# Optimization experiments

Measured on AMD Instinct MI355X. Metric: run time of the kernel, lower is better.

## Reference

```python
import jax, jax.numpy as jnp
import numpy as np

B, N, DIM = 2, 1024, 256
DEPTH, HEADS, DIM_HEAD = 4, 4, 64
INNER = HEADS * DIM_HEAD
SCALE = DIM_HEAD ** -0.5
STEP, LAMBD, EPS = 0.1, 0.1, 1e-5


def cx(re, im):
    return jax.lax.complex(re, im)


def setup_inputs() -> dict:
    key = jax.random.key(0)
    ks = jax.random.split(key, 8)
    s = np.float32(1.0 / np.sqrt(DIM))
    f32 = jnp.float32
    return {
        "x_re": jax.random.normal(ks[0], (B, N, DIM), f32),
        "x_im": jax.random.normal(ks[1], (B, N, DIM), f32),
        "ln1_w_re": jnp.ones((DEPTH, DIM), f32),
        "ln1_w_im": jnp.zeros((DEPTH, DIM), f32),
        "ln1_b_re": jnp.zeros((DEPTH, DIM), f32),
        "ln1_b_im": jnp.zeros((DEPTH, DIM), f32),
        "qkv_re": jax.random.normal(ks[2], (DEPTH, INNER, DIM), f32) * s,
        "qkv_im": jax.random.normal(ks[3], (DEPTH, INNER, DIM), f32) * s,
        "out_w_re": jax.random.normal(ks[4], (DEPTH, DIM, INNER), f32) * s,
        "out_w_im": jax.random.normal(ks[5], (DEPTH, DIM, INNER), f32) * s,
        "out_b_re": jnp.zeros((DEPTH, DIM), f32),
        "out_b_im": jnp.zeros((DEPTH, DIM), f32),
        "ln2_w_re": jnp.ones((DEPTH, DIM), f32),
        "ln2_w_im": jnp.zeros((DEPTH, DIM), f32),
        "ln2_b_re": jnp.zeros((DEPTH, DIM), f32),
        "ln2_b_im": jnp.zeros((DEPTH, DIM), f32),
        "ff_re": jax.random.normal(ks[6], (DEPTH, DIM, DIM), f32) * s,
        "ff_im": jax.random.normal(ks[7], (DEPTH, DIM, DIM), f32) * s,
    }


def complex_layernorm(x, w, b):
    # per-component mean/var on real and imag (torch unbiased=False), complex sqrt
    mean = cx(jnp.mean(x.real, -1, keepdims=True), jnp.mean(x.imag, -1, keepdims=True))
    var = cx(jnp.var(x.real, -1, keepdims=True), jnp.var(x.imag, -1, keepdims=True))
    xn = (x - mean) / jnp.sqrt(var + EPS)
    return w * xn + b


def attention(x, Wqkv, Wout, bout):
    # torch Linear: y = x @ W^T ; shared qkv projection w
    w = jnp.einsum('bnd,ed->bne', x, Wqkv)              # [B,N,INNER]
    w = w.reshape(B, N, HEADS, DIM_HEAD).transpose(0, 2, 1, 3)  # [B,H,N,Dh]
    dots = jnp.einsum('bhnd,bhmd->bhnm', w, w.conj()) * SCALE   # complex scores
    mag = jnp.abs(dots)
    a = jax.nn.softmax(mag, axis=-1)                    # softmax on magnitudes
    ph = jnp.angle(dots)                                # polar reconstruction
    attn = cx(a * jnp.cos(ph), a * jnp.sin(ph))
    out = jnp.einsum('bhnm,bhmd->bhnd', attn, w)
    out = out.transpose(0, 2, 1, 3).reshape(B, N, INNER)
    return jnp.einsum('bne,de->bnd', out, Wout) + bout


def feedforward(x, W):
    # FeedForward type1: x1 = x W^T ; CReLU(x + step*x1 - step*lambd)
    x1 = jnp.einsum('bnd,ed->bne', x, W)
    z = x + STEP * x1 - STEP * LAMBD
    return cx(jax.nn.relu(z.real), jax.nn.relu(z.imag))


def reference(x_re, x_im, ln1_w_re, ln1_w_im, ln1_b_re, ln1_b_im,
              qkv_re, qkv_im, out_w_re, out_w_im, out_b_re, out_b_im,
              ln2_w_re, ln2_w_im, ln2_b_re, ln2_b_im, ff_re, ff_im):
    x = cx(x_re, x_im)
    for l in range(DEPTH):
        xn = complex_layernorm(x, cx(ln1_w_re[l], ln1_w_im[l]), cx(ln1_b_re[l], ln1_b_im[l]))
        grad_x = attention(xn, cx(qkv_re[l], qkv_im[l]), cx(out_w_re[l], out_w_im[l]),
                           cx(out_b_re[l], out_b_im[l])) + x
        xn2 = complex_layernorm(grad_x, cx(ln2_w_re[l], ln2_w_im[l]), cx(ln2_b_re[l], ln2_b_im[l]))
        x = feedforward(xn2, cx(ff_re[l], ff_im[l]))
    return x
```

## Files before the change

kernel.cpp:

```cpp
#include <hip/hip_runtime.h>
#include <math.h>

#define B_ 2
#define N_ 1024
#define DIM_ 256
#define DEPTH_ 4
#define HEADS_ 4
#define DHEAD_ 64
#define INNER_ 256
#define SCALE_ 0.125f
#define STEP_ 0.1f
#define LAMBD_ 0.1f
#define EPS_ 1e-5f

typedef __attribute__((ext_vector_type(8))) short short8;
typedef __attribute__((ext_vector_type(4))) float f32x4;

__device__ __forceinline__ unsigned short bf16_rne(float x) {
    unsigned u = __float_as_uint(x);
    unsigned r = (u + 0x7FFFu + ((u >> 16) & 1u)) >> 16;
    return (unsigned short)r;
}
__device__ __forceinline__ float bf16_tof(unsigned short h) {
    return __uint_as_float(((unsigned)h) << 16);
}
__device__ __forceinline__ void split2(float x, unsigned short& hi, unsigned short& lo) {
    hi = bf16_rne(x);
    lo = bf16_rne(x - bf16_tof(hi));
}
__device__ __forceinline__ f32x4 mfma16(short8 a, short8 b, f32x4 c) {
    return __builtin_amdgcn_mfma_f32_16x16x32_bf16(a, b, c, 0, 0, 0);
}
__device__ __forceinline__ short8 neg8(short8 v) {
    union { short8 s; unsigned u[4]; } a; a.s = v;
    a.u[0] ^= 0x80008000u; a.u[1] ^= 0x80008000u;
    a.u[2] ^= 0x80008000u; a.u[3] ^= 0x80008000u;
    return a.s;
}

__global__ __launch_bounds__(64)
void ln_kernel(const float* __restrict__ xr, const float* __restrict__ xi,
               const float* __restrict__ wr, const float* __restrict__ wi,
               const float* __restrict__ br, const float* __restrict__ bi,
               float* __restrict__ outr, float* __restrict__ outi,
               unsigned short* __restrict__ planes, int S) {
    int row = blockIdx.x;
    int lane = threadIdx.x;
    int base = row * DIM_ + lane * 4;

    float4 xr4 = *(const float4*)(xr + base);
    float4 xi4 = *(const float4*)(xi + base);
    float ar[4] = {xr4.x, xr4.y, xr4.z, xr4.w};
    float ai[4] = {xi4.x, xi4.y, xi4.z, xi4.w};

    float sr = ar[0] + ar[1] + ar[2] + ar[3];
    float si = ai[0] + ai[1] + ai[2] + ai[3];
#pragma unroll
    for (int o = 1; o < 64; o <<= 1) {
        sr += __shfl_xor(sr, o, 64);
        si += __shfl_xor(si, o, 64);
    }
    float mre = sr * (1.f / DIM_), mim = si * (1.f / DIM_);

    float drv[4], div[4];
    float vr = 0.f, vi = 0.f;
#pragma unroll
    for (int j = 0; j < 4; j++) {
        drv[j] = ar[j] - mre;
        div[j] = ai[j] - mim;
        vr += drv[j] * drv[j];
        vi += div[j] * div[j];
    }
#pragma unroll
    for (int o = 1; o < 64; o <<= 1) {
        vr += __shfl_xor(vr, o, 64);
        vi += __shfl_xor(vi, o, 64);
    }
    float c = vr * (1.f / DIM_) + EPS_;
    float d = vi * (1.f / DIM_);
    float r = sqrtf(c * c + d * d);
    float sre = sqrtf(0.5f * (r + c));
    float sim = sqrtf(fmaxf(0.5f * (r - c), 0.f));
    float inv = 1.f / r;

    int wc = lane * 4;
    float4 wr4 = *(const float4*)(wr + wc);
    float4 wi4 = *(const float4*)(wi + wc);
    float4 br4 = *(const float4*)(br + wc);
    float4 bi4 = *(const float4*)(bi + wc);
    float wrv[4] = {wr4.x, wr4.y, wr4.z, wr4.w};
    float wiv[4] = {wi4.x, wi4.y, wi4.z, wi4.w};
    float brv[4] = {br4.x, br4.y, br4.z, br4.w};
    float biv[4] = {bi4.x, bi4.y, bi4.z, bi4.w};

    float orr[4], oii[4];
    unsigned short rh[4], rl[4], ih[4], il[4];
#pragma unroll
    for (int j = 0; j < 4; j++) {
        float nr = (drv[j] * sre + div[j] * sim) * inv;
        float ni = (div[j] * sre - drv[j] * sim) * inv;
        orr[j] = wrv[j] * nr - wiv[j] * ni + brv[j];
        oii[j] = wrv[j] * ni + wiv[j] * nr + biv[j];
        split2(orr[j], rh[j], rl[j]);
        split2(oii[j], ih[j], il[j]);
    }
    *(float4*)(outr + base) = make_float4(orr[0], orr[1], orr[2], orr[3]);
    *(float4*)(outi + base) = make_float4(oii[0], oii[1], oii[2], oii[3]);
    *(ushort4*)(planes + 0 * (size_t)S + base) = make_ushort4(rh[0], rh[1], rh[2], rh[3]);
    *(ushort4*)(planes + 1 * (size_t)S + base) = make_ushort4(rl[0], rl[1], rl[2], rl[3]);
    *(ushort4*)(planes + 2 * (size_t)S + base) = make_ushort4(ih[0], ih[1], ih[2], ih[3]);
    *(ushort4*)(planes + 3 * (size_t)S + base) = make_ushort4(il[0], il[1], il[2], il[3]);
}

__global__ void wsplit_all(const float* __restrict__ s0r, const float* __restrict__ s0i,
                           const float* __restrict__ s1r, const float* __restrict__ s1i,
                           const float* __restrict__ s2r, const float* __restrict__ s2i,
                           unsigned short* __restrict__ d0,
                           unsigned short* __restrict__ d1,
                           unsigned short* __restrict__ d2) {
    const int PER = DEPTH_ * 65536;
    int gid = blockIdx.x * 256 + threadIdx.x;
    int sel = gid / PER;
    int idx = gid - sel * PER;
    const float* wr = (sel == 0) ? s0r : (sel == 1) ? s1r : s2r;
    const float* wi = (sel == 0) ? s0i : (sel == 1) ? s1i : s2i;
    unsigned short* dst = (sel == 0) ? d0 : (sel == 1) ? d1 : d2;
    int l = idx >> 16, e = idx & 65535;
    unsigned short rh, rl, ih, il;
    split2(wr[idx], rh, rl);
    split2(wi[idx], ih, il);
    size_t base = (size_t)l * 4 * 65536;
    dst[base + 0 * 65536 + e] = rh;
    dst[base + 1 * 65536 + e] = rl;
    dst[base + 2 * 65536 + e] = ih;
    dst[base + 3 * 65536 + e] = il;
}

template <int MODE>
__global__ __launch_bounds__(256)
void gemm_mfma(const unsigned short* __restrict__ Ap, int aStride,
               const unsigned short* __restrict__ Bp,
               unsigned short* __restrict__ wpo, unsigned short* __restrict__ wtpo,
               const float* __restrict__ biasR, const float* __restrict__ biasI,
               const float* resR, const float* resI,
               float* xoR, float* xoI, int S) {
    __shared__ short8 Bs[2][4][4][64];
    const int K = 256;
    int tileM = blockIdx.x * 32, tileN = blockIdx.y * 64;
    int tid = threadIdx.x;
    int wave = tid >> 6, lane = tid & 63;
    int m16 = lane & 15, quad = lane >> 4;
    int rowHalf = wave & 1, ntBase = (wave >> 1) * 2;
    int rowA = tileM + rowHalf * 16 + m16;

    f32x4 accP[2], accN[2], accIa[2], accIb[2];
#pragma unroll
    for (int j = 0; j < 2; j++) {
        accP[j] = (f32x4){0,0,0,0}; accN[j] = (f32x4){0,0,0,0};
        accIa[j] = (f32x4){0,0,0,0}; accIb[j] = (f32x4){0,0,0,0};
    }

    int ls = lane;
    int lrow = tileN + (ls & 15);
    int lk0 = (ls >> 4) * 8;

    for (int k0 = 0; k0 < 256; k0 += 32) {
        int buf = (k0 >> 5) & 1;
#pragma unroll
        for (int nt = 0; nt < 4; nt++) {
            Bs[buf][wave][nt][ls] =
                *(const short8*)(Bp + (size_t)wave * 65536 + (size_t)(lrow + nt * 16) * K + k0 + lk0);
        }
        int kb = k0 + quad * 8;
        short8 a[4];
#pragma unroll
        for (int p = 0; p < 4; p++)
            a[p] = *(const short8*)(Ap + (size_t)p * aStride + (size_t)rowA * K + kb);
        __syncthreads();
#pragma unroll
        for (int j = 0; j < 2; j++) {
            int nt = ntBase + j;
            short8 b[4];
#pragma unroll
            for (int p = 0; p < 4; p++)
                b[p] = Bs[buf][p][nt][lane];
            accP[j]  = mfma16(a[0], b[0], accP[j]);
            accP[j]  = mfma16(a[0], b[1], accP[j]);
            accP[j]  = mfma16(a[1], b[0], accP[j]);
            accN[j]  = mfma16(a[2], b[2], accN[j]);
            accN[j]  = mfma16(a[2], b[3], accN[j]);
            accN[j]  = mfma16(a[3], b[2], accN[j]);
            accIa[j] = mfma16(a[0], b[2], accIa[j]);
            accIa[j] = mfma16(a[0], b[3], accIa[j]);
            accIa[j] = mfma16(a[1], b[2], accIa[j]);
            accIb[j] = mfma16(a[2], b[0], accIb[j]);
            accIb[j] = mfma16(a[2], b[1], accIb[j]);
            accIb[j] = mfma16(a[3], b[0], accIb[j]);
        }
    }

#pragma unroll
    for (int j = 0; j < 2; j++) {
        int nt = ntBase + j;
#pragma unroll
        for (int r = 0; r < 4; r++) {
            int row = tileM + rowHalf * 16 + quad * 4 + r;
            int col = tileN + nt * 16 + m16;
            size_t g = (size_t)row * 256 + col;
            float vr = accP[j][r] - accN[j][r];
            float vi = accIa[j][r] + accIb[j][r];
            if (MODE == 1) {
                unsigned short h0, h1, h2, h3;
                split2(vr, h0, h1);
                split2(vi, h2, h3);
                size_t tidx = ((size_t)(row >> 10) * 256 + col) * 1024 + (row & 1023);
                wpo[0 * (size_t)S + g] = h0;
                wpo[1 * (size_t)S + g] = h1;
                wpo[2 * (size_t)S + g] = h2;
                wpo[3 * (size_t)S + g] = h3;
                wtpo[0 * (size_t)S + tidx] = h0;
                wtpo[1 * (size_t)S + tidx] = h1;
                wtpo[2 * (size_t)S + tidx] = h2;
                wtpo[3 * (size_t)S + tidx] = h3;
            } else if (MODE == 2) {
                xoR[g] = vr + biasR[col] + resR[g];
                xoI[g] = vi + biasI[col] + resI[g];
            } else {
                float zr = resR[g] + STEP_ * vr - STEP_ * LAMBD_;
                float zi = resI[g] + STEP_ * vi;
                xoR[g] = fmaxf(zr, 0.f);
                xoI[g] = fmaxf(zi, 0.f);
            }
        }
    }
}

__global__ __launch_bounds__(256, 2)
void attn_mfma(const unsigned short* __restrict__ wp,
               const unsigned short* __restrict__ wtp,
               float* __restrict__ Op, float* __restrict__ ml, int S) {
    __shared__ unsigned int ShBuf[6336];
    __shared__ float mlbuf[4][64][2];

    int tid = threadIdx.x;
    int wave = tid >> 6, lane = tid & 63;
    int m16 = lane & 15, quad = lane >> 4;
    int zz = blockIdx.x, bb = zz >> 2, hh = zz & 3;
    int q0 = blockIdx.y * 16;
    int kz = blockIdx.z;

    short8 qf[4][2];
    {
        size_t qbase = (size_t)(bb * N_ + q0 + m16) * INNER_ + hh * DHEAD_;
#pragma unroll
        for (int p = 0; p < 4; p++)
#pragma unroll
            for (int kc = 0; kc < 2; kc++)
                qf[p][kc] = *(const short8*)(wp + (size_t)p * S + qbase + kc * 32 + quad * 8);
    }

    float mrow = -1e30f, lrow = 0.f;
    f32x4 Oa[4][2];
#pragma unroll
    for (int ni = 0; ni < 4; ni++) { Oa[ni][0] = (f32x4){0,0,0,0}; Oa[ni][1] = (f32x4){0,0,0,0}; }

    unsigned int* prbu = ShBuf + wave * 1056;

    for (int t = 0; t < 2; t++) {
        int kt = kz * 8 + wave + 4 * t;

        f32x4 sr[4], si[4];
#pragma unroll
        for (int ni = 0; ni < 4; ni++) { sr[ni] = (f32x4){0,0,0,0}; si[ni] = (f32x4){0,0,0,0}; }
#pragma unroll
        for (int ni = 0; ni < 4; ni++) {
            size_t kbase = (size_t)(bb * N_ + kt * 64 + ni * 16 + m16) * INNER_ + hh * DHEAD_;
            short8 kf[4][2];
#pragma unroll
            for (int p = 0; p < 4; p++)
#pragma unroll
                for (int kc = 0; kc < 2; kc++)
                    kf[p][kc] = *(const short8*)(wp + (size_t)p * S + kbase + kc * 32 + quad * 8);
#pragma unroll
            for (int kc = 0; kc < 2; kc++) {
                short8 nki_h = neg8(kf[2][kc]);
                short8 nki_l = neg8(kf[3][kc]);
                f32x4 r = sr[ni], im = si[ni];
                r  = mfma16(kf[0][kc], qf[0][kc], r);
                r  = mfma16(kf[0][kc], qf[1][kc], r);
                r  = mfma16(kf[1][kc], qf[0][kc], r);
                r  = mfma16(kf[2][kc], qf[2][kc], r);
                r  = mfma16(kf[2][kc], qf[3][kc], r);
                r  = mfma16(kf[3][kc], qf[2][kc], r);
                im = mfma16(kf[0][kc], qf[2][kc], im);
                im = mfma16(kf[0][kc], qf[3][kc], im);
                im = mfma16(kf[1][kc], qf[2][kc], im);
                im = mfma16(nki_h, qf[0][kc], im);
                im = mfma16(nki_h, qf[1][kc], im);
                im = mfma16(nki_l, qf[0][kc], im);
                sr[ni] = r; si[ni] = im;
            }
        }

        float mag[4][4], srs[4][4], sis[4][4];
        float mx = -1e30f;
#pragma unroll
        for (int ni = 0; ni < 4; ni++)
#pragma unroll
            for (int r = 0; r < 4; r++) {
                float a = sr[ni][r] * SCALE_, b = si[ni][r] * SCALE_;
                srs[ni][r] = a; sis[ni][r] = b;
                float mg = sqrtf(a * a + b * b);
                mag[ni][r] = mg;
                mx = fmaxf(mx, mg);
            }
        mx = fmaxf(mx, __shfl_xor(mx, 16, 64));
        mx = fmaxf(mx, __shfl_xor(mx, 32, 64));
        float newm = fmaxf(mrow, mx);
        float alpha = __expf(mrow - newm);
        mrow = newm;
        float psum = 0.f;
#pragma unroll
        for (int ni = 0; ni < 4; ni++)
#pragma unroll
            for (int r = 0; r < 4; r++) {
                float p = __expf(mag[ni][r] - newm);
                psum += p;
                float sc = (mag[ni][r] > 0.f) ? (p / mag[ni][r]) : 0.f;
                float pr = (mag[ni][r] > 0.f) ? srs[ni][r] * sc : p;
                float pi = sis[ni][r] * sc;
                int key = ni * 16 + quad * 4 + r;
                prbu[m16 * 66 + key] = ((unsigned)bf16_rne(pi) << 16) | bf16_rne(pr);
            }
        psum += __shfl_xor(psum, 16, 64);
        psum += __shfl_xor(psum, 32, 64);
        lrow = lrow * alpha + psum;
#pragma unroll
        for (int ni = 0; ni < 4; ni++)
#pragma unroll
            for (int r = 0; r < 4; r++) { Oa[ni][0][r] *= alpha; Oa[ni][1][r] *= alpha; }

        short8 prh[2], pih[2], nih[2];
#pragma unroll
        for (int kc = 0; kc < 2; kc++) {
            short8 x, y;
#pragma unroll
            for (int j = 0; j < 8; j++) {
                unsigned val = prbu[m16 * 66 + kc * 32 + quad * 8 + j];
                x[j] = (short)(val & 0xffffu);
                y[j] = (short)(val >> 16);
            }
            prh[kc] = x; pih[kc] = y; nih[kc] = neg8(y);
        }

#pragma unroll
        for (int ni = 0; ni < 4; ni++) {
            size_t vbase = (size_t)(bb * INNER_ + hh * DHEAD_ + ni * 16 + m16) * N_ + kt * 64;
            short8 vr0 = *(const short8*)(wtp + 0 * (size_t)S + vbase + quad * 8);
            short8 vr1 = *(const short8*)(wtp + 0 * (size_t)S + vbase + 32 + quad * 8);
            short8 vi0 = *(const short8*)(wtp + 2 * (size_t)S + vbase + quad * 8);
            short8 vi1 = *(const short8*)(wtp + 2 * (size_t)S + vbase + 32 + quad * 8);
            f32x4 orv = Oa[ni][0], oiv = Oa[ni][1];
            orv = mfma16(vr0, prh[0], orv);
            orv = mfma16(vi0, nih[0], orv);
            orv = mfma16(vr1, prh[1], orv);
            orv = mfma16(vi1, nih[1], orv);
            oiv = mfma16(vr0, pih[0], oiv);
            oiv = mfma16(vi0, prh[0], oiv);
            oiv = mfma16(vr1, pih[1], oiv);
            oiv = mfma16(vi1, prh[1], oiv);
            Oa[ni][0] = orv; Oa[ni][1] = oiv;
        }
    }

    float* Obuf = (float*)ShBuf;
    __syncthreads();
    if (wave != 0) {
        float* mb = Obuf + (wave - 1) * 2112 + lane * 33;
#pragma unroll
        for (int ni = 0; ni < 4; ni++)
#pragma unroll
            for (int r = 0; r < 4; r++) {
                mb[ni * 8 + r]     = Oa[ni][0][r];
                mb[ni * 8 + 4 + r] = Oa[ni][1][r];
            }
        mlbuf[wave][lane][0] = mrow;
        mlbuf[wave][lane][1] = lrow;
    }
    __syncthreads();
    if (wave == 0) {
        float mm = mrow;
#pragma unroll
        for (int w = 1; w < 4; w++) mm = fmaxf(mm, mlbuf[w][lane][0]);
        float a0 = __expf(mrow - mm);
        float ltot = a0 * lrow;
        float aw[3];
#pragma unroll
        for (int w = 1; w < 4; w++) {
            aw[w - 1] = __expf(mlbuf[w][lane][0] - mm);
            ltot += aw[w - 1] * mlbuf[w][lane][1];
        }
        size_t obase = (size_t)(bb * N_ + q0 + m16) * INNER_ + hh * DHEAD_;
        float* opr = Op + (size_t)kz * 2 * S;
        float* opi = opr + S;
#pragma unroll
        for (int ni = 0; ni < 4; ni++)
#pragma unroll
            for (int r = 0; r < 4; r++) {
                float vr = a0 * Oa[ni][0][r];
                float vi = a0 * Oa[ni][1][r];
#pragma unroll
                for (int w = 1; w < 4; w++) {
                    vr += aw[w - 1] * Obuf[(w - 1) * 2112 + lane * 33 + ni * 8 + r];
                    vi += aw[w - 1] * Obuf[(w - 1) * 2112 + lane * 33 + ni * 8 + 4 + r];
                }
                size_t o = obase + ni * 16 + quad * 4 + r;
                opr[o] = vr;
                opi[o] = vi;
            }
        if (quad == 0) {
            int row = bb * N_ + q0 + m16;
            ((float2*)ml)[kz * 8192 + row * 4 + hh] = make_float2(mm, ltot);
        }
    }
}

__global__ void attn_merge(const float* __restrict__ Op, const float* __restrict__ ml,
                           unsigned short* __restrict__ aop, int S) {
    int idx = blockIdx.x * 256 + threadIdx.x;
    int row = idx >> 8;
    int hh = (idx >> 6) & 3;
    float2 ml0 = ((const float2*)ml)[row * 4 + hh];
    float2 ml1 = ((const float2*)ml)[8192 + row * 4 + hh];
    float mm = fmaxf(ml0.x, ml1.x);
    float a0 = __expf(ml0.x - mm), a1 = __expf(ml1.x - mm);
    float invl = 1.f / (a0 * ml0.y + a1 * ml1.y);
    float vr = (a0 * Op[idx] + a1 * Op[2 * (size_t)S + idx]) * invl;
    float vi = (a0 * Op[(size_t)S + idx] + a1 * Op[3 * (size_t)S + idx]) * invl;
    unsigned short h0, h1, h2, h3;
    split2(vr, h0, h1);
    split2(vi, h2, h3);
    aop[0 * (size_t)S + idx] = h0;
    aop[1 * (size_t)S + idx] = h1;
    aop[2 * (size_t)S + idx] = h2;
    aop[3 * (size_t)S + idx] = h3;
}

__global__ void pack_real(const float* __restrict__ xr, float* __restrict__ out, int cap) {
    int idx = blockIdx.x * 256 + threadIdx.x;
    if (idx < cap) out[idx] = xr[idx];
}

extern "C" void kernel_launch(void* const* d_in, const int* in_sizes, int n_in,
                              void* d_out, int out_size, void* d_ws, size_t ws_size,
                              hipStream_t stream) {
    const float* in_xre = (const float*)d_in[0];
    const float* in_xim = (const float*)d_in[1];
    const float* ln1wr = (const float*)d_in[2];
    const float* ln1wi = (const float*)d_in[3];
    const float* ln1br = (const float*)d_in[4];
    const float* ln1bi = (const float*)d_in[5];
    const float* qkvr  = (const float*)d_in[6];
    const float* qkvi  = (const float*)d_in[7];
    const float* outwr = (const float*)d_in[8];
    const float* outwi = (const float*)d_in[9];
    const float* outbr = (const float*)d_in[10];
    const float* outbi = (const float*)d_in[11];
    const float* ln2wr = (const float*)d_in[12];
    const float* ln2wi = (const float*)d_in[13];
    const float* ln2br = (const float*)d_in[14];
    const float* ln2bi = (const float*)d_in[15];
    const float* ffr   = (const float*)d_in[16];
    const float* ffi   = (const float*)d_in[17];

    const size_t S = (size_t)B_ * N_ * DIM_;
    const int    Si = (int)S;

    float* ws  = (float*)d_ws;
    float* xre = ws;            float* xim = xre + S;
    float* xnr = xim + S;       float* xni = xnr + S;
    float* Opart = xni + S;
    float* mlb   = Opart + 4 * S;

    unsigned short* xnp   = (unsigned short*)(mlb + 32768);
    unsigned short* aop   = xnp + 4 * S;
    unsigned short* wpb   = aop + 4 * S;
    unsigned short* wtpb  = wpb + 4 * S;
    unsigned short* qkvp  = wtpb + 4 * S;
    unsigned short* outwp = qkvp + (size_t)DEPTH_ * 4 * 65536;
    unsigned short* ffp   = outwp + (size_t)DEPTH_ * 4 * 65536;

    wsplit_all<<<3 * DEPTH_ * 65536 / 256, 256, 0, stream>>>(
        qkvr, qkvi, outwr, outwi, ffr, ffi, qkvp, outwp, ffp);

    const int MR = B_ * N_;
    dim3 gGemm(MR / 32, INNER_ / 64);
    dim3 gAttn(B_ * HEADS_, N_ / 16, 2);
    int eBlocks = (int)(S / 256);

    bool directOut = (out_size >= (int)(2 * S));
    float* foutR = directOut ? (float*)d_out : xre;
    float* foutI = directOut ? (float*)d_out + S : xim;

    for (int l = 0; l < DEPTH_; l++) {
        const float* xinR = (l == 0) ? in_xre : xre;
        const float* xinI = (l == 0) ? in_xim : xim;

        ln_kernel<<<MR, 64, 0, stream>>>(xinR, xinI,
            ln1wr + l * DIM_, ln1wi + l * DIM_, ln1br + l * DIM_, ln1bi + l * DIM_,
            xnr, xni, xnp, Si);

        gemm_mfma<1><<<gGemm, 256, 0, stream>>>(xnp, Si, qkvp + (size_t)l * 4 * 65536,
            wpb, wtpb, nullptr, nullptr, nullptr, nullptr, nullptr, nullptr, Si);

        attn_mfma<<<gAttn, 256, 0, stream>>>(wpb, wtpb, Opart, mlb, Si);
        attn_merge<<<eBlocks, 256, 0, stream>>>(Opart, mlb, aop, Si);

        gemm_mfma<2><<<gGemm, 256, 0, stream>>>(aop, Si, outwp + (size_t)l * 4 * 65536,
            nullptr, nullptr, outbr + l * DIM_, outbi + l * DIM_, xinR, xinI, xre, xim, Si);

        ln_kernel<<<MR, 64, 0, stream>>>(xre, xim,
            ln2wr + l * DIM_, ln2wi + l * DIM_, ln2br + l * DIM_, ln2bi + l * DIM_,
            xnr, xni, xnp, Si);

        float* oR = (l == DEPTH_ - 1) ? foutR : xre;
        float* oI = (l == DEPTH_ - 1) ? foutI : xim;
        gemm_mfma<3><<<gGemm, 256, 0, stream>>>(xnp, Si, ffp + (size_t)l * 4 * 65536,
            nullptr, nullptr, nullptr, nullptr, xnr, xni, oR, oI, Si);
    }

    if (!directOut) {
        pack_real<<<eBlocks, 256, 0, stream>>>(xre, (float*)d_out, out_size);
    }
}
```

Measured before the change: 526.4 us.

## Split attention key range four ways and drop per-wave online softmax loop

The attention kernel now splits the key dimension into four chunks across grid z instead of two, so each wave handles a single 64-key tile and no longer needs the two-iteration online-softmax rescaling loop. The merge kernel combines four partial outputs and max/sum pairs, and the workspace grows to hold them. This doubles the block count for more parallelism and less per-block serial work, at the cost of more partial-output traffic in the merge step.

New measurement: 551.6 us. 1.05x slower.

```diff
diff --git a/kernel.cpp b/kernel.cpp
--- a/kernel.cpp
+++ b/kernel.cpp
@@ -248,6 +248,7 @@
     int zz = blockIdx.x, bb = zz >> 2, hh = zz & 3;
     int q0 = blockIdx.y * 16;
     int kz = blockIdx.z;
+    int kt = kz * 4 + wave;
 
     short8 qf[4][2];
     {
@@ -259,118 +260,106 @@
                 qf[p][kc] = *(const short8*)(wp + (size_t)p * S + qbase + kc * 32 + quad * 8);
     }
 
-    float mrow = -1e30f, lrow = 0.f;
+    unsigned int* prbu = ShBuf + wave * 1056;
+
+    f32x4 sr[4], si[4];
+#pragma unroll
+    for (int ni = 0; ni < 4; ni++) { sr[ni] = (f32x4){0,0,0,0}; si[ni] = (f32x4){0,0,0,0}; }
+#pragma unroll
+    for (int ni = 0; ni < 4; ni++) {
+        size_t kbase = (size_t)(bb * N_ + kt * 64 + ni * 16 + m16) * INNER_ + hh * DHEAD_;
+        short8 kf[4][2];
+#pragma unroll
+        for (int p = 0; p < 4; p++)
+#pragma unroll
+            for (int kc = 0; kc < 2; kc++)
+                kf[p][kc] = *(const short8*)(wp + (size_t)p * S + kbase + kc * 32 + quad * 8);
+#pragma unroll
+        for (int kc = 0; kc < 2; kc++) {
+            short8 nki_h = neg8(kf[2][kc]);
+            short8 nki_l = neg8(kf[3][kc]);
+            f32x4 r = sr[ni], im = si[ni];
+            r  = mfma16(kf[0][kc], qf[0][kc], r);
+            r  = mfma16(kf[0][kc], qf[1][kc], r);
+            r  = mfma16(kf[1][kc], qf[0][kc], r);
+            r  = mfma16(kf[2][kc], qf[2][kc], r);
+            r  = mfma16(kf[2][kc], qf[3][kc], r);
+            r  = mfma16(kf[3][kc], qf[2][kc], r);
+            im = mfma16(kf[0][kc], qf[2][kc], im);
+            im = mfma16(kf[0][kc], qf[3][kc], im);
+            im = mfma16(kf[1][kc], qf[2][kc], im);
+            im = mfma16(nki_h, qf[0][kc], im);
+            im = mfma16(nki_h, qf[1][kc], im);
+            im = mfma16(nki_l, qf[0][kc], im);
+            sr[ni] = r; si[ni] = im;
+        }
+    }
+
+    float mag[4][4];
+    float mx = -1e30f;
+#pragma unroll
+    for (int ni = 0; ni < 4; ni++)
+#pragma unroll
+        for (int r = 0; r < 4; r++) {
+            float a = sr[ni][r] * SCALE_, b = si[ni][r] * SCALE_;
+            sr[ni][r] = a; si[ni][r] = b;
+            float mg = sqrtf(a * a + b * b);
+            mag[ni][r] = mg;
+            mx = fmaxf(mx, mg);
+        }
+    mx = fmaxf(mx, __shfl_xor(mx, 16, 64));
+    mx = fmaxf(mx, __shfl_xor(mx, 32, 64));
+    float psum = 0.f;
+#pragma unroll
+    for (int ni = 0; ni < 4; ni++)
+#pragma unroll
+        for (int r = 0; r < 4; r++) {
+            float p = __expf(mag[ni][r] - mx);
+            psum += p;
+            float mg = mag[ni][r];
+            float sc = (mg > 0.f) ? (p / mg) : 0.f;
+            float pr = (mg > 0.f) ? sr[ni][r] * sc : p;
+            float pi = si[ni][r] * sc;
+            int key = ni * 16 + quad * 4 + r;
+            prbu[m16 * 66 + key] = ((unsigned)bf16_rne(pi) << 16) | bf16_rne(pr);
+        }
+    psum += __shfl_xor(psum, 16, 64);
+    psum += __shfl_xor(psum, 32, 64);
+    float mrow = mx, lrow = psum;
+
+    short8 prh[2], pih[2], nih[2];
+#pragma unroll
+    for (int kc = 0; kc < 2; kc++) {
+        short8 x, y;
+#pragma unroll
+        for (int j = 0; j < 8; j++) {
+            unsigned val = prbu[m16 * 66 + kc * 32 + quad * 8 + j];
+            x[j] = (short)(val & 0xffffu);
+            y[j] = (short)(val >> 16);
+        }
+        prh[kc] = x; pih[kc] = y; nih[kc] = neg8(y);
+    }
+
     f32x4 Oa[4][2];
 #pragma unroll
     for (int ni = 0; ni < 4; ni++) { Oa[ni][0] = (f32x4){0,0,0,0}; Oa[ni][1] = (f32x4){0,0,0,0}; }
-
-    unsigned int* prbu = ShBuf + wave * 1056;
-
-    for (int t = 0; t < 2; t++) {
-        int kt = kz * 8 + wave + 4 * t;
-
-        f32x4 sr[4], si[4];
-#pragma unroll
-        for (int ni = 0; ni < 4; ni++) { sr[ni] = (f32x4){0,0,0,0}; si[ni] = (f32x4){0,0,0,0}; }
-#pragma unroll
-        for (int ni = 0; ni < 4; ni++) {
-            size_t kbase = (size_t)(bb * N_ + kt * 64 + ni * 16 + m16) * INNER_ + hh * DHEAD_;
-            short8 kf[4][2];
-#pragma unroll
-            for (int p = 0; p < 4; p++)
-#pragma unroll
-                for (int kc = 0; kc < 2; kc++)
-                    kf[p][kc] = *(const short8*)(wp + (size_t)p * S + kbase + kc * 32 + quad * 8);
-#pragma unroll
-            for (int kc = 0; kc < 2; kc++) {
-                short8 nki_h = neg8(kf[2][kc]);
-                short8 nki_l = neg8(kf[3][kc]);
-                f32x4 r = sr[ni], im = si[ni];
-                r  = mfma16(kf[0][kc], qf[0][kc], r);
-                r  = mfma16(kf[0][kc], qf[1][kc], r);
-                r  = mfma16(kf[1][kc], qf[0][kc], r);
-                r  = mfma16(kf[2][kc], qf[2][kc], r);
-                r  = mfma16(kf[2][kc], qf[3][kc], r);
-                r  = mfma16(kf[3][kc], qf[2][kc], r);
-                im = mfma16(kf[0][kc], qf[2][kc], im);
-                im = mfma16(kf[0][kc], qf[3][kc], im);
-                im = mfma16(kf[1][kc], qf[2][kc], im);
-                im = mfma16(nki_h, qf[0][kc], im);
-                im = mfma16(nki_h, qf[1][kc], im);
-                im = mfma16(nki_l, qf[0][kc], im);
-                sr[ni] = r; si[ni] = im;
-            }
-        }
-
-        float mag[4][4], srs[4][4], sis[4][4];
-        float mx = -1e30f;
-#pragma unroll
-        for (int ni = 0; ni < 4; ni++)
-#pragma unroll
-            for (int r = 0; r < 4; r++) {
-                float a = sr[ni][r] * SCALE_, b = si[ni][r] * SCALE_;
-                srs[ni][r] = a; sis[ni][r] = b;
-                float mg = sqrtf(a * a + b * b);
-                mag[ni][r] = mg;
-                mx = fmaxf(mx, mg);
-            }
-        mx = fmaxf(mx, __shfl_xor(mx, 16, 64));
-        mx = fmaxf(mx, __shfl_xor(mx, 32, 64));
-        float newm = fmaxf(mrow, mx);
-        float alpha = __expf(mrow - newm);
-        mrow = newm;
-        float psum = 0.f;
-#pragma unroll
-        for (int ni = 0; ni < 4; ni++)
-#pragma unroll
-            for (int r = 0; r < 4; r++) {
-                float p = __expf(mag[ni][r] - newm);
-                psum += p;
-                float sc = (mag[ni][r] > 0.f) ? (p / mag[ni][r]) : 0.f;
-                float pr = (mag[ni][r] > 0.f) ? srs[ni][r] * sc : p;
-                float pi = sis[ni][r] * sc;
-                int key = ni * 16 + quad * 4 + r;
-                prbu[m16 * 66 + key] = ((unsigned)bf16_rne(pi) << 16) | bf16_rne(pr);
-            }
-        psum += __shfl_xor(psum, 16, 64);
-        psum += __shfl_xor(psum, 32, 64);
-        lrow = lrow * alpha + psum;
-#pragma unroll
-        for (int ni = 0; ni < 4; ni++)
-#pragma unroll
-            for (int r = 0; r < 4; r++) { Oa[ni][0][r] *= alpha; Oa[ni][1][r] *= alpha; }
-
-        short8 prh[2], pih[2], nih[2];
-#pragma unroll
-        for (int kc = 0; kc < 2; kc++) {
-            short8 x, y;
-#pragma unroll
-            for (int j = 0; j < 8; j++) {
-                unsigned val = prbu[m16 * 66 + kc * 32 + quad * 8 + j];
-                x[j] = (short)(val & 0xffffu);
-                y[j] = (short)(val >> 16);
-            }
-            prh[kc] = x; pih[kc] = y; nih[kc] = neg8(y);
-        }
-
-#pragma unroll
-        for (int ni = 0; ni < 4; ni++) {
-            size_t vbase = (size_t)(bb * INNER_ + hh * DHEAD_ + ni * 16 + m16) * N_ + kt * 64;
-            short8 vr0 = *(const short8*)(wtp + 0 * (size_t)S + vbase + quad * 8);
-            short8 vr1 = *(const short8*)(wtp + 0 * (size_t)S + vbase + 32 + quad * 8);
-            short8 vi0 = *(const short8*)(wtp + 2 * (size_t)S + vbase + quad * 8);
-            short8 vi1 = *(const short8*)(wtp + 2 * (size_t)S + vbase + 32 + quad * 8);
-            f32x4 orv = Oa[ni][0], oiv = Oa[ni][1];
-            orv = mfma16(vr0, prh[0], orv);
-            orv = mfma16(vi0, nih[0], orv);
-            orv = mfma16(vr1, prh[1], orv);
-            orv = mfma16(vi1, nih[1], orv);
-            oiv = mfma16(vr0, pih[0], oiv);
-            oiv = mfma16(vi0, prh[0], oiv);
-            oiv = mfma16(vr1, pih[1], oiv);
-            oiv = mfma16(vi1, prh[1], oiv);
-            Oa[ni][0] = orv; Oa[ni][1] = oiv;
-        }
+#pragma unroll
+    for (int ni = 0; ni < 4; ni++) {
+        size_t vbase = (size_t)(bb * INNER_ + hh * DHEAD_ + ni * 16 + m16) * N_ + kt * 64;
+        short8 vr0 = *(const short8*)(wtp + 0 * (size_t)S + vbase + quad * 8);
+        short8 vr1 = *(const short8*)(wtp + 0 * (size_t)S + vbase + 32 + quad * 8);
+        short8 vi0 = *(const short8*)(wtp + 2 * (size_t)S + vbase + quad * 8);
+        short8 vi1 = *(const short8*)(wtp + 2 * (size_t)S + vbase + 32 + quad * 8);
+        f32x4 orv = Oa[ni][0], oiv = Oa[ni][1];
+        orv = mfma16(vr0, prh[0], orv);
+        orv = mfma16(vi0, nih[0], orv);
+        orv = mfma16(vr1, prh[1], orv);
+        orv = mfma16(vi1, nih[1], orv);
+        oiv = mfma16(vr0, pih[0], oiv);
+        oiv = mfma16(vi0, prh[0], oiv);
+        oiv = mfma16(vr1, pih[1], oiv);
+        oiv = mfma16(vi1, prh[1], oiv);
+        Oa[ni][0] = orv; Oa[ni][1] = oiv;
     }
 
     float* Obuf = (float*)ShBuf;
@@ -430,13 +419,24 @@
     int idx = blockIdx.x * 256 + threadIdx.x;
     int row = idx >> 8;
     int hh = (idx >> 6) & 3;
-    float2 ml0 = ((const float2*)ml)[row * 4 + hh];
-    float2 ml1 = ((const float2*)ml)[8192 + row * 4 + hh];
-    float mm = fmaxf(ml0.x, ml1.x);
-    float a0 = __expf(ml0.x - mm), a1 = __expf(ml1.x - mm);
-    float invl = 1.f / (a0 * ml0.y + a1 * ml1.y);
-    float vr = (a0 * Op[idx] + a1 * Op[2 * (size_t)S + idx]) * invl;
-    float vi = (a0 * Op[(size_t)S + idx] + a1 * Op[3 * (size_t)S + idx]) * invl;
+    float2 mq[4];
+#pragma unroll
+    for (int q = 0; q < 4; q++) mq[q] = ((const float2*)ml)[q * 8192 + row * 4 + hh];
+    float mm = fmaxf(fmaxf(mq[0].x, mq[1].x), fmaxf(mq[2].x, mq[3].x));
+    float aq[4], ltot = 0.f;
+#pragma unroll
+    for (int q = 0; q < 4; q++) {
+        aq[q] = __expf(mq[q].x - mm);
+        ltot += aq[q] * mq[q].y;
+    }
+    float invl = 1.f / ltot;
+    float vr = 0.f, vi = 0.f;
+#pragma unroll
+    for (int q = 0; q < 4; q++) {
+        vr += aq[q] * Op[(size_t)q * 2 * S + idx];
+        vi += aq[q] * Op[(size_t)q * 2 * S + S + idx];
+    }
+    vr *= invl; vi *= invl;
     unsigned short h0, h1, h2, h3;
     split2(vr, h0, h1);
     split2(vi, h2, h3);
@@ -480,9 +480,9 @@
     float* xre = ws;            float* xim = xre + S;
     float* xnr = xim + S;       float* xni = xnr + S;
     float* Opart = xni + S;
-    float* mlb   = Opart + 4 * S;
-
-    unsigned short* xnp   = (unsigned short*)(mlb + 32768);
+    float* mlb   = Opart + 8 * S;
+
+    unsigned short* xnp   = (unsigned short*)(mlb + 65536);
     unsigned short* aop   = xnp + 4 * S;
     unsigned short* wpb   = aop + 4 * S;
     unsigned short* wtpb  = wpb + 4 * S;
@@ -495,7 +495,7 @@
 
     const int MR = B_ * N_;
     dim3 gGemm(MR / 32, INNER_ / 64);
-    dim3 gAttn(B_ * HEADS_, N_ / 16, 2);
+    dim3 gAttn(B_ * HEADS_, N_ / 16, 4);
     int eBlocks = (int)(S / 256);
 
     bool directOut = (out_size >= (int)(2 * S));
```
